# Optimization experiments

Measured on AMD Instinct MI355X. Metric: run time of the kernel, lower is better.

## Reference

```python
import jax, jax.numpy as jnp
import numpy as np


def setup_inputs() -> dict:
    key = jax.random.key(0)
    k1, k2 = jax.random.split(key)
    N, D = 8192, 1024
    anchor = jax.random.normal(k1, (N, D), dtype=jnp.float32)
    negative = jax.random.normal(k2, (N, D), dtype=jnp.float32)
    return {"anchor": anchor, "negative": negative}


def reference(anchor, negative):
    # MSE(a, n) = mean((a - n)^2) over D = (||a||^2 + ||n||^2 - 2 a.n) / D
    D = anchor.shape[-1]
    a2 = jnp.sum(anchor * anchor, axis=-1, keepdims=True)      # [N, 1]
    n2 = jnp.sum(negative * negative, axis=-1)                  # [N]
    dots = jnp.einsum('id,jd->ij', anchor, negative)            # [N, N]
    mse = (a2 + n2[None, :] - 2.0 * dots) / D                   # [N, N]
    idx = jnp.argmax(mse, axis=1)                               # hardest negative per anchor
    return negative[idx]
```

## Files before the change

kernel.cpp:

```cpp
#include <hip/hip_runtime.h>
#include <hip/hip_bf16.h>
#include <stdint.h>

#define NROWS 8192
#define DIM   1024

typedef __attribute__((ext_vector_type(4))) int    i32x4;
typedef __attribute__((ext_vector_type(4))) float  f32x4;

__device__ __forceinline__ unsigned int f32_key(float val) {
    unsigned int b = __float_as_uint(val);
    b ^= (unsigned int)(((int)b >> 31) | 0x80000000);
    return b;
}
__device__ __forceinline__ float key_val(unsigned long long k) {
    unsigned int b = (unsigned int)(k >> 32);
    b = (b & 0x80000000u) ? (b ^ 0x80000000u) : ~b;
    return __uint_as_float(b);
}
__device__ __forceinline__ void load_lds16(const void* g, void* l) {
    __builtin_amdgcn_global_load_lds((const __attribute__((address_space(1))) void*)g,
                                     (__attribute__((address_space(3))) void*)l, 16, 0, 0);
}

__global__ __launch_bounds__(256) void prep_i8_kernel(const float* __restrict__ A,
                                                      const float* __restrict__ B,
                                                      signed char* __restrict__ Aq,
                                                      signed char* __restrict__ Bq,
                                                      float* __restrict__ fA,
                                                      float* __restrict__ fB,
                                                      float* __restrict__ a2,
                                                      float* __restrict__ n2) {
    const float* src = blockIdx.y ? B : A;
    signed char* qdst = blockIdx.y ? Bq : Aq;
    float* fdst = blockIdx.y ? fB : fA;
    float* sdst = blockIdx.y ? n2 : a2;
    int row  = blockIdx.x * 4 + (threadIdx.x >> 6);
    int lane = threadIdx.x & 63;
    const float* p = src + (size_t)row * DIM;

    float4 v[4];
    double s = 0.0;
    float mx = 0.0f;
#pragma unroll
    for (int q = 0; q < 4; ++q) {
        v[q] = *reinterpret_cast<const float4*>(p + (size_t)(lane + 64 * q) * 4);
        s += (double)v[q].x * v[q].x + (double)v[q].y * v[q].y +
             (double)v[q].z * v[q].z + (double)v[q].w * v[q].w;
        mx = fmaxf(mx, fmaxf(fmaxf(fabsf(v[q].x), fabsf(v[q].y)),
                             fmaxf(fabsf(v[q].z), fabsf(v[q].w))));
    }
#pragma unroll
    for (int m = 32; m >= 1; m >>= 1) {
        s  += __shfl_xor(s, m, 64);
        mx  = fmaxf(mx, __shfl_xor(mx, m, 64));
    }
    mx = fmaxf(mx, 1e-30f);
    const float scale = 127.0f / mx;
#pragma unroll
    for (int q = 0; q < 4; ++q) {
        int q0 = (int)rintf(v[q].x * scale);
        int q1 = (int)rintf(v[q].y * scale);
        int q2 = (int)rintf(v[q].z * scale);
        int q3 = (int)rintf(v[q].w * scale);
        int packed = (q0 & 0xFF) | ((q1 & 0xFF) << 8) | ((q2 & 0xFF) << 16) | (q3 << 24);
        *reinterpret_cast<int*>(qdst + (size_t)row * DIM + (size_t)(lane + 64 * q) * 4) = packed;
    }
    if (lane == 0) { sdst[row] = (float)s; fdst[row] = mx / 127.0f; }
}

__global__ __launch_bounds__(256, 4) void mfma_i8_kernel(
        const signed char* __restrict__ Aq,
        const signed char* __restrict__ Bq,
        const float* __restrict__ fA, const float* __restrict__ fB,
        const float* __restrict__ a2, const float* __restrict__ n2,
        unsigned long long* __restrict__ cand ) {
    __shared__ signed char lds[2][128 * 64];

    const int tid  = threadIdx.x;
    const int w    = tid >> 6;
    const int lane = tid & 63;
    const int row0 = blockIdx.x * 128;
    const int col0 = blockIdx.y * 128;
    const int wr = w >> 1, wc = w & 1;
    const int g = lane >> 4, m = lane & 15;

    i32x4 acc[4][4];
#pragma unroll
    for (int r = 0; r < 4; ++r)
#pragma unroll
        for (int c = 0; c < 4; ++c) acc[r][c] = (i32x4)0;

    const signed char* gA = Aq + (size_t)row0 * DIM;
    const signed char* gB = Bq + (size_t)col0 * DIM;

    for (int kt = 0; kt < DIM; kt += 64) {
#pragma unroll
        for (int p = 0; p < 2; ++p) {
            int li  = p * 256 + tid;
            int row = li >> 2;
            int ck  = li & 3;
            int cg  = ck ^ ((row >> 1) & 3);
            load_lds16(gA + (size_t)row * DIM + kt + cg * 16,
                       (char*)&lds[0][0] + (size_t)li * 16);
            load_lds16(gB + (size_t)row * DIM + kt + cg * 16,
                       (char*)&lds[1][0] + (size_t)li * 16);
        }
        __syncthreads();
        {
            i32x4 af[4], bf[4];
#pragma unroll
            for (int r = 0; r < 4; ++r) {
                int arow = wr * 64 + r * 16 + m;
                int ch   = g ^ ((arow >> 1) & 3);
                af[r] = *(const i32x4*)((const char*)&lds[0][0] + arow * 64 + ch * 16);
                int brow = wc * 64 + r * 16 + m;
                int ch2  = g ^ ((brow >> 1) & 3);
                bf[r] = *(const i32x4*)((const char*)&lds[1][0] + brow * 64 + ch2 * 16);
            }
#pragma unroll
            for (int r = 0; r < 4; ++r)
#pragma unroll
                for (int c = 0; c < 4; ++c)
                    acc[r][c] = __builtin_amdgcn_mfma_i32_16x16x64_i8(af[r], bf[c], acc[r][c], 0, 0, 0);
        }
        __syncthreads();
    }

    const int colbase = col0 + wc * 64;
    const int cb = blockIdx.y * 2 + wc;
    float n2v[4], fbv[4];
#pragma unroll
    for (int c = 0; c < 4; ++c) {
        n2v[c] = n2[colbase + c * 16 + m];
        fbv[c] = fB[colbase + c * 16 + m];
    }
#pragma unroll
    for (int r = 0; r < 4; ++r) {
#pragma unroll
        for (int j = 0; j < 4; ++j) {
            int row = row0 + wr * 64 + r * 16 + g * 4 + j;
            float arow = a2[row];
            float far  = fA[row];
            unsigned long long k1 = 0ull, k2 = 0ull;
#pragma unroll
            for (int c = 0; c < 4; ++c) {
                int col = colbase + c * 16 + m;
                float dot = (float)acc[r][c][j] * far * fbv[c];
                float t = arow + n2v[c];
                t = t - 2.0f * dot;
                float val = t * (1.0f / 1024.0f);
                unsigned long long key =
                    ((unsigned long long)f32_key(val) << 32) |
                    (unsigned long long)(0xFFFFFFFFu - (unsigned)col);
                if (key > k1) { k2 = k1; k1 = key; } else if (key > k2) { k2 = key; }
            }
#pragma unroll
            for (int s = 1; s < 16; s <<= 1) {
                unsigned long long o1 = __shfl_xor(k1, s, 64);
                unsigned long long o2 = __shfl_xor(k2, s, 64);
                unsigned long long hi = k1 > o1 ? k1 : o1;
                unsigned long long md = k1 > o1 ? o1 : k1;
                unsigned long long l2 = k2 > o2 ? k2 : o2;
                k1 = hi; k2 = md > l2 ? md : l2;
            }
            if (m == 0) {
                unsigned long long* p = &cand[((size_t)row * 128 + cb) * 2];
                p[0] = k1; p[1] = k2;
            }
        }
    }
}

#define DELTA 1.5e-2f
__global__ __launch_bounds__(256) void refine_gather_kernel(
        const float* __restrict__ A, const float* __restrict__ B,
        const float* __restrict__ a2, const float* __restrict__ n2,
        const unsigned long long* __restrict__ cand,
        float* __restrict__ out) {
    int row  = blockIdx.x * 4 + (threadIdx.x >> 6);
    int lane = threadIdx.x & 63;
    const unsigned long long* cp = cand + (size_t)row * 256;

    unsigned long long k[4];
#pragma unroll
    for (int q = 0; q < 4; ++q) k[q] = cp[lane + 64 * q];

    unsigned long long mx = k[0];
#pragma unroll
    for (int q = 1; q < 4; ++q) if (k[q] > mx) mx = k[q];
#pragma unroll
    for (int s = 1; s < 64; s <<= 1) {
        unsigned long long o = __shfl_xor(mx, s, 64);
        if (o > mx) mx = o;
    }
    const float thr = key_val(mx) - DELTA;

    const float* ap = A + (size_t)row * DIM;
    const double a2row = (double)a2[row];
    double bestv = -1.0e300;
    int    bestc = 0x7FFFFFFF;

#pragma unroll
    for (int q = 0; q < 4; ++q) {
        float kv = key_val(k[q]);
        int   kc = (int)(0xFFFFFFFFu - (unsigned int)(k[q] & 0xFFFFFFFFull));
        unsigned long long mask = __ballot(kv >= thr);
        while (mask) {
            int src = __ffsll((long long)mask) - 1;
            mask &= mask - 1;
            int col = __shfl(kc, src, 64);
            const float* bp = B + (size_t)col * DIM;
            double part = 0.0;
#pragma unroll
            for (int u = 0; u < 4; ++u) {
                float4 va = reinterpret_cast<const float4*>(ap)[lane + 64 * u];
                float4 vb = reinterpret_cast<const float4*>(bp)[lane + 64 * u];
                part += (double)va.x * vb.x + (double)va.y * vb.y +
                        (double)va.z * vb.z + (double)va.w * vb.w;
            }
#pragma unroll
            for (int s = 1; s < 64; s <<= 1) part += __shfl_xor(part, s, 64);
            double val = (a2row + (double)n2[col] - 2.0 * part) * (1.0 / 1024.0);
            if (val > bestv || (val == bestv && col < bestc)) { bestv = val; bestc = col; }
        }
    }

    const float4* srcp = reinterpret_cast<const float4*>(B + (size_t)bestc * DIM);
    float4*       dstp = reinterpret_cast<float4*>(out + (size_t)row * DIM);
#pragma unroll
    for (int u = 0; u < 4; ++u) dstp[lane + 64 * u] = srcp[lane + 64 * u];
}

__global__ __launch_bounds__(256) void sumsq_kernel(const float* __restrict__ A,
                                                    const float* __restrict__ B,
                                                    float* __restrict__ a2,
                                                    float* __restrict__ n2) {
    const float* src = (blockIdx.y == 0) ? A : B;
    float*       dst = (blockIdx.y == 0) ? a2 : n2;
    int row  = blockIdx.x * 4 + (threadIdx.x >> 6);
    int lane = threadIdx.x & 63;
    const float* p = src + (size_t)row * DIM;
    double s = 0.0;
#pragma unroll
    for (int q = 0; q < 4; ++q) {
        float4 v = *reinterpret_cast<const float4*>(p + (size_t)(lane + 64 * q) * 4);
        s += (double)v.x * v.x + (double)v.y * v.y + (double)v.z * v.z + (double)v.w * v.w;
    }
#pragma unroll
    for (int m = 32; m >= 1; m >>= 1) s += __shfl_xor(s, m, 64);
    if (lane == 0) dst[row] = (float)s;
}

__global__ __launch_bounds__(256) void mse_argmax_kernel(
        const float* __restrict__ A, const float* __restrict__ B,
        const float* __restrict__ a2, const float* __restrict__ n2,
        unsigned long long* __restrict__ best) {
    __shared__ float As[16][132];
    __shared__ float Bs[16][132];
    const int tid = threadIdx.x;
    const int tx = tid & 15, ty = tid >> 4;
    const int row0 = blockIdx.x * 128;
    const int col0 = blockIdx.y * 128;
    float acc[8][8];
#pragma unroll
    for (int r = 0; r < 8; ++r)
#pragma unroll
        for (int c = 0; c < 8; ++c) acc[r][c] = 0.0f;
    for (int kt = 0; kt < DIM; kt += 16) {
#pragma unroll
        for (int p = 0; p < 2; ++p) {
            int li = p * 256 + tid;
            int r  = li >> 2;
            int s4 = li & 3;
            float4 va = *reinterpret_cast<const float4*>(&A[(size_t)(row0 + r) * DIM + kt + s4 * 4]);
            float4 vb = *reinterpret_cast<const float4*>(&B[(size_t)(col0 + r) * DIM + kt + s4 * 4]);
            As[s4 * 4 + 0][r] = va.x; As[s4 * 4 + 1][r] = va.y;
            As[s4 * 4 + 2][r] = va.z; As[s4 * 4 + 3][r] = va.w;
            Bs[s4 * 4 + 0][r] = vb.x; Bs[s4 * 4 + 1][r] = vb.y;
            Bs[s4 * 4 + 2][r] = vb.z; Bs[s4 * 4 + 3][r] = vb.w;
        }
        __syncthreads();
#pragma unroll
        for (int kk = 0; kk < 16; ++kk) {
            float af[8], bfv[8];
#pragma unroll
            for (int r = 0; r < 8; ++r) af[r] = As[kk][ty + 16 * r];
#pragma unroll
            for (int c = 0; c < 8; ++c) bfv[c] = Bs[kk][tx + 16 * c];
#pragma unroll
            for (int r = 0; r < 8; ++r)
#pragma unroll
                for (int c = 0; c < 8; ++c) acc[r][c] = fmaf(af[r], bfv[c], acc[r][c]);
        }
        __syncthreads();
    }
#pragma unroll
    for (int r = 0; r < 8; ++r) {
        const int row = row0 + ty + 16 * r;
        const float arow = a2[row];
        unsigned long long bestk = 0ull;
#pragma unroll
        for (int c = 0; c < 8; ++c) {
            const int col = col0 + tx + 16 * c;
            float t = arow + n2[col];
            t = t - 2.0f * acc[r][c];
            const float val = t * (1.0f / 1024.0f);
            unsigned long long key =
                ((unsigned long long)f32_key(val) << 32) |
                (unsigned long long)(0xFFFFFFFFu - (unsigned)col);
            if (key > bestk) bestk = key;
        }
#pragma unroll
        for (int mm = 1; mm < 16; mm <<= 1) {
            unsigned long long other = __shfl_xor(bestk, mm, 16);
            if (other > bestk) bestk = other;
        }
        if (tx == 0) atomicMax(&best[row], bestk);
    }
}

__global__ __launch_bounds__(256) void gather_kernel(
        const float* __restrict__ B,
        const unsigned long long* __restrict__ best,
        float* __restrict__ out) {
    const int row = blockIdx.x;
    const unsigned int col = 0xFFFFFFFFu - (unsigned int)(best[row] & 0xFFFFFFFFull);
    const float4* src = reinterpret_cast<const float4*>(B + (size_t)col * DIM);
    float4*       dst = reinterpret_cast<float4*>(out + (size_t)row * DIM);
    dst[threadIdx.x] = src[threadIdx.x];
}

extern "C" void kernel_launch(void* const* d_in, const int* in_sizes, int n_in,
                              void* d_out, int out_size, void* d_ws, size_t ws_size,
                              hipStream_t stream) {
    const float* anchor   = (const float*)d_in[0];
    const float* negative = (const float*)d_in[1];
    float* out = (float*)d_out;
    char* ws = (char*)d_ws;

    const size_t qplane    = (size_t)NROWS * DIM;
    const size_t candBytes = (size_t)NROWS * 256 * sizeof(unsigned long long);
    const size_t SC        = 32768;
    const size_t need_i8   = 2 * qplane + 4 * SC + candBytes;

    if (ws_size >= need_i8) {
        signed char* Aq = (signed char*)(ws);
        signed char* Bq = (signed char*)(ws + qplane);
        float* fA = (float*)(ws + 2 * qplane);
        float* fB = (float*)(ws + 2 * qplane + SC);
        float* a2 = (float*)(ws + 2 * qplane + 2 * SC);
        float* n2 = (float*)(ws + 2 * qplane + 3 * SC);
        unsigned long long* cand = (unsigned long long*)(ws + 2 * qplane + 4 * SC);

        prep_i8_kernel<<<dim3(NROWS / 4, 2), 256, 0, stream>>>(
            anchor, negative, Aq, Bq, fA, fB, a2, n2);
        mfma_i8_kernel<<<dim3(NROWS / 128, NROWS / 128), 256, 0, stream>>>(
            Aq, Bq, fA, fB, a2, n2, cand);
        refine_gather_kernel<<<NROWS / 4, 256, 0, stream>>>(
            anchor, negative, a2, n2, cand, out);
    } else {
        float* a2 = (float*)(ws);
        float* n2 = (float*)(ws + 32768);
        unsigned long long* best = (unsigned long long*)(ws + 65536);
        hipMemsetAsync(best, 0, NROWS * sizeof(unsigned long long), stream);
        sumsq_kernel<<<dim3(NROWS / 4, 2), 256, 0, stream>>>(anchor, negative, a2, n2);
        mse_argmax_kernel<<<dim3(NROWS / 128, NROWS / 128), 256, 0, stream>>>(anchor, negative, a2, n2, best);
        gather_kernel<<<NROWS, 256, 0, stream>>>(negative, best, out);
    }
}
```

Measured before the change: 166.5 us.

## Enlarge int8 GEMM tile to 256x256 with triple-buffered LDS pipeline and XCD-aware mapping

The int8 MFMA candidate kernel moves from 128x128 tiles with 256 threads and a single-buffered LDS loop to 256x256 tiles with 512 threads. It uses a three-stage LDS ring filled by async global-to-LDS loads, split into two half-phases with waitcnt and barriers, plus s_setprio around the MFMA bursts. Blocks are remapped so that neighbouring row tiles land on the same XCD for L2 reuse. The aim is to hide global load latency and cut redundant global traffic, at the cost of 96KB LDS, more accumulator registers and lower occupancy. The candidate index cb changes to bx*4+wcol, which stays within the same 128 column-block slots per row.

```diff
diff --git a/kernel.cpp b/kernel.cpp
--- a/kernel.cpp
+++ b/kernel.cpp
@@ -69,66 +69,114 @@
     if (lane == 0) { sdst[row] = (float)s; fdst[row] = mx / 127.0f; }
 }
 
-__global__ __launch_bounds__(256, 4) void mfma_i8_kernel(
+__global__ __launch_bounds__(512, 2) void mfma_i8_kernel(
         const signed char* __restrict__ Aq,
         const signed char* __restrict__ Bq,
         const float* __restrict__ fA, const float* __restrict__ fB,
         const float* __restrict__ a2, const float* __restrict__ n2,
         unsigned long long* __restrict__ cand ) {
-    __shared__ signed char lds[2][128 * 64];
+    __shared__ __attribute__((aligned(16))) char lds_raw[98304];
 
     const int tid  = threadIdx.x;
-    const int w    = tid >> 6;
+    const int wid  = tid >> 6;
     const int lane = tid & 63;
-    const int row0 = blockIdx.x * 128;
-    const int col0 = blockIdx.y * 128;
-    const int wr = w >> 1, wc = w & 1;
+    const int wr   = wid >> 2;
+    const int wcol = wid & 3;
     const int g = lane >> 4, m = lane & 15;
 
-    i32x4 acc[4][4];
-#pragma unroll
-    for (int r = 0; r < 4; ++r)
+    const int bid   = blockIdx.x;
+    const int xcd   = bid & 7;
+    const int local = bid >> 3;
+    const int by    = xcd * 4 + (local & 3);
+    const int bx    = local >> 2;
+    const int brow  = by * 256;
+    const int bcol  = bx * 256;
+
+    const signed char* gA = Aq + (size_t)brow * DIM;
+    const signed char* gB = Bq + (size_t)bcol * DIM;
+
+    i32x4 acc[8][4];
+#pragma unroll
+    for (int r = 0; r < 8; ++r)
 #pragma unroll
         for (int c = 0; c < 4; ++c) acc[r][c] = (i32x4)0;
 
-    const signed char* gA = Aq + (size_t)row0 * DIM;
-    const signed char* gB = Bq + (size_t)col0 * DIM;
-
-    for (int kt = 0; kt < DIM; kt += 64) {
+    auto stage_half = [&](int t, int h) {
+        char* base = lds_raw + (size_t)(t % 3) * 32768 + (size_t)h * 16384;
+        const signed char* gp = (h ? gB : gA) + t * 64;
 #pragma unroll
         for (int p = 0; p < 2; ++p) {
-            int li  = p * 256 + tid;
+            int li  = p * 512 + tid;
             int row = li >> 2;
             int ck  = li & 3;
             int cg  = ck ^ ((row >> 1) & 3);
-            load_lds16(gA + (size_t)row * DIM + kt + cg * 16,
-                       (char*)&lds[0][0] + (size_t)li * 16);
-            load_lds16(gB + (size_t)row * DIM + kt + cg * 16,
-                       (char*)&lds[1][0] + (size_t)li * 16);
-        }
-        __syncthreads();
-        {
-            i32x4 af[4], bf[4];
-#pragma unroll
-            for (int r = 0; r < 4; ++r) {
-                int arow = wr * 64 + r * 16 + m;
-                int ch   = g ^ ((arow >> 1) & 3);
-                af[r] = *(const i32x4*)((const char*)&lds[0][0] + arow * 64 + ch * 16);
-                int brow = wc * 64 + r * 16 + m;
-                int ch2  = g ^ ((brow >> 1) & 3);
-                bf[r] = *(const i32x4*)((const char*)&lds[1][0] + brow * 64 + ch2 * 16);
-            }
-#pragma unroll
-            for (int r = 0; r < 4; ++r)
-#pragma unroll
-                for (int c = 0; c < 4; ++c)
-                    acc[r][c] = __builtin_amdgcn_mfma_i32_16x16x64_i8(af[r], bf[c], acc[r][c], 0, 0, 0);
-        }
-        __syncthreads();
-    }
-
-    const int colbase = col0 + wc * 64;
-    const int cb = blockIdx.y * 2 + wc;
+            load_lds16(gp + (size_t)row * DIM + cg * 16, base + (size_t)li * 16);
+        }
+    };
+
+    stage_half(0, 0); stage_half(0, 1);
+    stage_half(1, 0); stage_half(1, 1);
+
+    for (int t = 0; t < 16; ++t) {
+        if (t < 15) { asm volatile("s_waitcnt vmcnt(4)" ::: "memory"); }
+        else        { asm volatile("s_waitcnt vmcnt(0)" ::: "memory"); }
+        __builtin_amdgcn_sched_barrier(0);
+        __builtin_amdgcn_s_barrier();
+        __builtin_amdgcn_sched_barrier(0);
+
+        const char* la = lds_raw + (size_t)(t % 3) * 32768;
+        const char* lb = la + 16384;
+
+        i32x4 af[4], bf[4];
+#pragma unroll
+        for (int rl = 0; rl < 4; ++rl) {
+            int arow = wr * 128 + rl * 16 + m;
+            int ch   = g ^ ((arow >> 1) & 3);
+            af[rl] = *(const i32x4*)(la + arow * 64 + ch * 16);
+        }
+#pragma unroll
+        for (int nf = 0; nf < 4; ++nf) {
+            int brw = wcol * 64 + nf * 16 + m;
+            int ch2 = g ^ ((brw >> 1) & 3);
+            bf[nf] = *(const i32x4*)(lb + brw * 64 + ch2 * 16);
+        }
+        if (t + 2 < 16) stage_half(t + 2, 0);
+        __builtin_amdgcn_s_barrier();
+        asm volatile("s_waitcnt lgkmcnt(0)" ::: "memory");
+        __builtin_amdgcn_sched_barrier(0);
+        __builtin_amdgcn_s_setprio(1);
+#pragma unroll
+        for (int rl = 0; rl < 4; ++rl)
+#pragma unroll
+            for (int nf = 0; nf < 4; ++nf)
+                acc[rl][nf] = __builtin_amdgcn_mfma_i32_16x16x64_i8(af[rl], bf[nf], acc[rl][nf], 0, 0, 0);
+        __builtin_amdgcn_s_setprio(0);
+        __builtin_amdgcn_sched_barrier(0);
+        __builtin_amdgcn_s_barrier();
+
+        i32x4 af2[4];
+#pragma unroll
+        for (int rl = 0; rl < 4; ++rl) {
+            int arow = wr * 128 + (4 + rl) * 16 + m;
+            int ch   = g ^ ((arow >> 1) & 3);
+            af2[rl] = *(const i32x4*)(la + arow * 64 + ch * 16);
+        }
+        if (t + 2 < 16) stage_half(t + 2, 1);
+        __builtin_amdgcn_s_barrier();
+        asm volatile("s_waitcnt lgkmcnt(0)" ::: "memory");
+        __builtin_amdgcn_sched_barrier(0);
+        __builtin_amdgcn_s_setprio(1);
+#pragma unroll
+        for (int rl = 0; rl < 4; ++rl)
+#pragma unroll
+            for (int nf = 0; nf < 4; ++nf)
+                acc[4 + rl][nf] = __builtin_amdgcn_mfma_i32_16x16x64_i8(af2[rl], bf[nf], acc[4 + rl][nf], 0, 0, 0);
+        __builtin_amdgcn_s_setprio(0);
+        __builtin_amdgcn_sched_barrier(0);
+    }
+
+    const int colbase = bcol + wcol * 64;
+    const int cb = bx * 4 + wcol;
     float n2v[4], fbv[4];
 #pragma unroll
     for (int c = 0; c < 4; ++c) {
@@ -136,20 +184,20 @@
         fbv[c] = fB[colbase + c * 16 + m];
     }
 #pragma unroll
-    for (int r = 0; r < 4; ++r) {
+    for (int rf = 0; rf < 8; ++rf) {
 #pragma unroll
         for (int j = 0; j < 4; ++j) {
-            int row = row0 + wr * 64 + r * 16 + g * 4 + j;
+            int row = brow + wr * 128 + rf * 16 + g * 4 + j;
             float arow = a2[row];
             float far  = fA[row];
             unsigned long long k1 = 0ull, k2 = 0ull;
 #pragma unroll
             for (int c = 0; c < 4; ++c) {
                 int col = colbase + c * 16 + m;
-                float dot = (float)acc[r][c][j] * far * fbv[c];
-                float t = arow + n2v[c];
-                t = t - 2.0f * dot;
-                float val = t * (1.0f / 1024.0f);
+                float dot = (float)acc[rf][c][j] * far * fbv[c];
+                float tt = arow + n2v[c];
+                tt = tt - 2.0f * dot;
+                float val = tt * (1.0f / 1024.0f);
                 unsigned long long key =
                     ((unsigned long long)f32_key(val) << 32) |
                     (unsigned long long)(0xFFFFFFFFu - (unsigned)col);
@@ -355,7 +403,7 @@
 
         prep_i8_kernel<<<dim3(NROWS / 4, 2), 256, 0, stream>>>(
             anchor, negative, Aq, Bq, fA, fB, a2, n2);
-        mfma_i8_kernel<<<dim3(NROWS / 128, NROWS / 128), 256, 0, stream>>>(
+        mfma_i8_kernel<<<dim3((NROWS / 256) * (NROWS / 256)), 512, 0, stream>>>(
             Aq, Bq, fA, fB, a2, n2, cand);
         refine_gather_kernel<<<NROWS / 4, 256, 0, stream>>>(
             anchor, negative, a2, n2, cand, out);
```

Measured after the change: 169.4 us. No clear change (+1.7%).

## Double-buffer LDS tiles in int8 MFMA GEMM to overlap loads with compute

Applied to the files above, without the earlier changes.

Splits the shared-memory staging buffer into two halves and fully unrolls the K loop so the next 64-wide K slice is loaded into one buffer while MFMAs consume the other. This removes one barrier per iteration and aims to hide global-to-LDS latency behind matrix math. LDS per block doubles to 32 KB, which may limit occupancy at four blocks per CU, and correctness depends on the single barrier being enough to order the async LDS loads.

```diff
diff --git a/kernel.cpp b/kernel.cpp
--- a/kernel.cpp
+++ b/kernel.cpp
@@ -75,7 +75,7 @@
         const float* __restrict__ fA, const float* __restrict__ fB,
         const float* __restrict__ a2, const float* __restrict__ n2,
         unsigned long long* __restrict__ cand ) {
-    __shared__ signed char lds[2][128 * 64];
+    __shared__ signed char lds[2][2][128 * 64];
 
     const int tid  = threadIdx.x;
     const int w    = tid >> 6;
@@ -94,38 +94,73 @@
     const signed char* gA = Aq + (size_t)row0 * DIM;
     const signed char* gB = Bq + (size_t)col0 * DIM;
 
-    for (int kt = 0; kt < DIM; kt += 64) {
-#pragma unroll
-        for (int p = 0; p < 2; ++p) {
-            int li  = p * 256 + tid;
-            int row = li >> 2;
-            int ck  = li & 3;
-            int cg  = ck ^ ((row >> 1) & 3);
-            load_lds16(gA + (size_t)row * DIM + kt + cg * 16,
-                       (char*)&lds[0][0] + (size_t)li * 16);
-            load_lds16(gB + (size_t)row * DIM + kt + cg * 16,
-                       (char*)&lds[1][0] + (size_t)li * 16);
-        }
-        __syncthreads();
-        {
-            i32x4 af[4], bf[4];
-#pragma unroll
-            for (int r = 0; r < 4; ++r) {
-                int arow = wr * 64 + r * 16 + m;
-                int ch   = g ^ ((arow >> 1) & 3);
-                af[r] = *(const i32x4*)((const char*)&lds[0][0] + arow * 64 + ch * 16);
-                int brow = wc * 64 + r * 16 + m;
-                int ch2  = g ^ ((brow >> 1) & 3);
-                bf[r] = *(const i32x4*)((const char*)&lds[1][0] + brow * 64 + ch2 * 16);
-            }
-#pragma unroll
-            for (int r = 0; r < 4; ++r)
-#pragma unroll
-                for (int c = 0; c < 4; ++c)
-                    acc[r][c] = __builtin_amdgcn_mfma_i32_16x16x64_i8(af[r], bf[c], acc[r][c], 0, 0, 0);
-        }
-        __syncthreads();
-    }
+    const int li0 = tid, li1 = 256 + tid;
+    const int sr0 = li0 >> 2, sc0 = (li0 & 3) ^ ((sr0 >> 1) & 3);
+    const int sr1 = li1 >> 2, sc1 = (li1 & 3) ^ ((sr1 >> 1) & 3);
+    const signed char* srcA0 = gA + (size_t)sr0 * DIM + sc0 * 16;
+    const signed char* srcA1 = gA + (size_t)sr1 * DIM + sc1 * 16;
+    const signed char* srcB0 = gB + (size_t)sr0 * DIM + sc0 * 16;
+    const signed char* srcB1 = gB + (size_t)sr1 * DIM + sc1 * 16;
+    char* dA0b0 = (char*)&lds[0][0][0] + (size_t)li0 * 16;
+    char* dA1b0 = (char*)&lds[0][0][0] + (size_t)li1 * 16;
+    char* dB0b0 = (char*)&lds[0][1][0] + (size_t)li0 * 16;
+    char* dB1b0 = (char*)&lds[0][1][0] + (size_t)li1 * 16;
+    char* dA0b1 = (char*)&lds[1][0][0] + (size_t)li0 * 16;
+    char* dA1b1 = (char*)&lds[1][0][0] + (size_t)li1 * 16;
+    char* dB0b1 = (char*)&lds[1][1][0] + (size_t)li0 * 16;
+    char* dB1b1 = (char*)&lds[1][1][0] + (size_t)li1 * 16;
+
+#define STAGE0(OFF) { load_lds16(srcA0 + (OFF), dA0b0); load_lds16(srcA1 + (OFF), dA1b0); \
+                      load_lds16(srcB0 + (OFF), dB0b0); load_lds16(srcB1 + (OFF), dB1b0); }
+#define STAGE1(OFF) { load_lds16(srcA0 + (OFF), dA0b1); load_lds16(srcA1 + (OFF), dA1b1); \
+                      load_lds16(srcB0 + (OFF), dB0b1); load_lds16(srcB1 + (OFF), dB1b1); }
+
+    int offA[4], offB[4];
+#pragma unroll
+    for (int r = 0; r < 4; ++r) {
+        int arow = wr * 64 + r * 16 + m;
+        offA[r] = arow * 64 + (g ^ ((arow >> 1) & 3)) * 16;
+        int brow = wc * 64 + r * 16 + m;
+        offB[r] = brow * 64 + (g ^ ((brow >> 1) & 3)) * 16;
+    }
+    const char* laB0 = (const char*)&lds[0][0][0];
+    const char* lbB0 = (const char*)&lds[0][1][0];
+    const char* laB1 = (const char*)&lds[1][0][0];
+    const char* lbB1 = (const char*)&lds[1][1][0];
+
+    auto compute = [&](const char* la, const char* lb) {
+        i32x4 af[4], bf[4];
+#pragma unroll
+        for (int r = 0; r < 4; ++r) {
+            af[r] = *(const i32x4*)(la + offA[r]);
+            bf[r] = *(const i32x4*)(lb + offB[r]);
+        }
+#pragma unroll
+        for (int r = 0; r < 4; ++r)
+#pragma unroll
+            for (int c = 0; c < 4; ++c)
+                acc[r][c] = __builtin_amdgcn_mfma_i32_16x16x64_i8(af[r], bf[c], acc[r][c], 0, 0, 0);
+    };
+
+    STAGE0(0);   __syncthreads();
+    STAGE1(64);  compute(laB0, lbB0); __syncthreads();
+    STAGE0(128); compute(laB1, lbB1); __syncthreads();
+    STAGE1(192); compute(laB0, lbB0); __syncthreads();
+    STAGE0(256); compute(laB1, lbB1); __syncthreads();
+    STAGE1(320); compute(laB0, lbB0); __syncthreads();
+    STAGE0(384); compute(laB1, lbB1); __syncthreads();
+    STAGE1(448); compute(laB0, lbB0); __syncthreads();
+    STAGE0(512); compute(laB1, lbB1); __syncthreads();
+    STAGE1(576); compute(laB0, lbB0); __syncthreads();
+    STAGE0(640); compute(laB1, lbB1); __syncthreads();
+    STAGE1(704); compute(laB0, lbB0); __syncthreads();
+    STAGE0(768); compute(laB1, lbB1); __syncthreads();
+    STAGE1(832); compute(laB0, lbB0); __syncthreads();
+    STAGE0(896); compute(laB1, lbB1); __syncthreads();
+    STAGE1(960); compute(laB0, lbB0); __syncthreads();
+    compute(laB1, lbB1);
+#undef STAGE0
+#undef STAGE1
 
     const int colbase = col0 + wc * 64;
     const int cb = blockIdx.y * 2 + wc;
```

New measurement: 167.9 us. Within noise of the previous version (+0.8%).
